# Kernel optimization log

Measured on AMD Instinct MI355X. Metric: run time of the kernel, lower is better.

The kernel has to match this reference:

```python
import jax, jax.numpy as jnp
import numpy as np

EPS = 1e-8
LN_EPS = 1e-5
CAPACITY_BETA = 1.5
IDEAL_CLASSES = 5.0

B, F, E, H, C, G = 8192, 1024, 30, 256, 100, 4096


def setup_inputs() -> dict:
    key = jax.random.key(0)
    ks = jax.random.split(key, 8)
    x = jax.random.normal(ks[0], (B, F), dtype=jnp.float32)
    prototypes = jax.random.normal(ks[1], (E, F), dtype=jnp.float32)
    g_new = jax.random.normal(ks[2], (G,), dtype=jnp.float32)
    g_mem = jax.random.normal(ks[3], (E, G), dtype=jnp.float32)
    class_counts = jax.random.randint(ks[4], (E,), 0, 12, dtype=jnp.int32)
    W1 = jax.random.normal(ks[5], (E, F, H), dtype=jnp.float32) * (1.0 / np.sqrt(F))
    b1 = jnp.zeros((E, H), dtype=jnp.float32)
    gamma = jnp.ones((E, H), dtype=jnp.float32)
    beta = jnp.zeros((E, H), dtype=jnp.float32)
    W2 = jax.random.normal(ks[6], (E, H, C), dtype=jnp.float32) * (1.0 / np.sqrt(H))
    b2 = jnp.zeros((E, C), dtype=jnp.float32)
    return {"x": x, "prototypes": prototypes, "g_new": g_new, "g_mem": g_mem,
            "class_counts": class_counts, "W1": W1, "b1": b1, "gamma": gamma,
            "beta": beta, "W2": W2, "b2": b2}


def _route_scores(x, prototypes, g_new, g_mem, class_counts):
    # Cosine similarity of each sample to each expert prototype: [B, E]
    xn = x / (jnp.linalg.norm(x, axis=-1, keepdims=True) + EPS)
    pn = prototypes / (jnp.linalg.norm(prototypes, axis=-1, keepdims=True) + EPS)
    sim = xn @ pn.T
    # Gradient alignment score per expert (cosine of new grad vs EMA memory), mapped to [0, 1]
    gn = g_new / (jnp.linalg.norm(g_new) + EPS)
    gm = g_mem / (jnp.linalg.norm(g_mem, axis=-1, keepdims=True) + EPS)
    align = 0.5 * (1.0 + gm @ gn)  # [E]
    # Capacity penalty: exponential decay once an expert exceeds its ideal class load
    overload = jnp.maximum(class_counts.astype(jnp.float32) / IDEAL_CLASSES - 1.0, 0.0)
    capacity = jnp.exp(-CAPACITY_BETA * overload)  # [E]
    return sim * (align * capacity)[None, :]  # [B, E]


def reference(x, prototypes, g_new, g_mem, class_counts, W1, b1, gamma, beta, W2, b2):
    scores = _route_scores(x, prototypes, g_new, g_mem, class_counts)  # [B, E]
    assign = jnp.argmax(scores, axis=-1)  # [B] expert id per sample
    # Expert MLP: Linear -> LayerNorm -> GELU -> Linear, evaluated for all experts
    h = jnp.einsum('bf,efh->ebh', x, W1) + b1[:, None, :]  # [E, B, H]
    mu = h.mean(axis=-1, keepdims=True)
    var = ((h - mu) ** 2).mean(axis=-1, keepdims=True)
    ln = (h - mu) * jax.lax.rsqrt(var + LN_EPS) * gamma[:, None, :] + beta[:, None, :]
    a = jax.nn.gelu(ln, approximate=False)  # torch nn.GELU default is exact erf
    logits_all = jnp.einsum('ebh,ehc->ebc', a, W2) + b2[:, None, :]  # [E, B, C]
    # Dispatch: each sample keeps only its assigned expert's logits
    logits = logits_all[assign, jnp.arange(x.shape[0])]  # [B, C]
    return logits
```

## Files before the change

### kernel.cpp

```cpp
#include <hip/hip_runtime.h>
#include <hip/hip_bf16.h>
#include <math.h>
#include <float.h>

namespace {
constexpr int Bn = 8192;
constexpr int Fn = 1024;
constexpr int En = 30;
constexpr int Hn = 256;
constexpr int Cn = 100;
constexpr int Gn = 4096;
constexpr int TILECAP64 = 158;
constexpr int TILECAP16 = 540;
constexpr float EPSF  = 1e-8f;
constexpr float LNEPS = 1e-5f;

typedef _Float16 f16x8 __attribute__((ext_vector_type(8)));
typedef float    f32x4 __attribute__((ext_vector_type(4)));

__device__ __forceinline__ int bswz(int k) { return (k & 7) ^ ((k >> 3) << 2); }
}

#define GLDS16(g, s) __builtin_amdgcn_global_load_lds(                         \
    (const __attribute__((address_space(1))) void*)(uintptr_t)(g),             \
    (__attribute__((address_space(3))) void*)(uintptr_t)(s), 16, 0, 0)

__global__ __launch_bounds__(256) void k_route_w(
    const float* __restrict__ protos,
    const float* __restrict__ g_new,
    const float* __restrict__ g_mem,
    const int* __restrict__ ccounts,
    float* __restrict__ w,
    int* __restrict__ cnt) {
  const int e = blockIdx.x, t = threadIdx.x;
  if (e == 0 && t < 32) cnt[t] = 0;
  float d = 0.f, gm2 = 0.f, gn2 = 0.f, p2 = 0.f;
  for (int g = t; g < Gn; g += 256) {
    float a = g_new[g];
    float m = g_mem[(size_t)e * Gn + g];
    d += a * m; gm2 += m * m; gn2 += a * a;
  }
  for (int f = t; f < Fn; f += 256) {
    float v = protos[(size_t)e * Fn + f];
    p2 += v * v;
  }
#pragma unroll
  for (int m = 1; m < 64; m <<= 1) {
    d   += __shfl_xor(d, m);
    gm2 += __shfl_xor(gm2, m);
    gn2 += __shfl_xor(gn2, m);
    p2  += __shfl_xor(p2, m);
  }
  __shared__ float red[4][4];
  const int lane = t & 63, wid = t >> 6;
  if (lane == 0) { red[wid][0] = d; red[wid][1] = gm2; red[wid][2] = gn2; red[wid][3] = p2; }
  __syncthreads();
  if (t == 0) {
    d   = red[0][0] + red[1][0] + red[2][0] + red[3][0];
    gm2 = red[0][1] + red[1][1] + red[2][1] + red[3][1];
    gn2 = red[0][2] + red[1][2] + red[2][2] + red[3][2];
    p2  = red[0][3] + red[1][3] + red[2][3] + red[3][3];
    float align = 0.5f * (1.0f + d / ((sqrtf(gm2) + EPSF) * (sqrtf(gn2) + EPSF)));
    float over  = fmaxf((float)ccounts[e] / 5.0f - 1.0f, 0.0f);
    float cap   = expf(-1.5f * over);
    w[e] = align * cap / (sqrtf(p2) + EPSF);
  }
}

__global__ __launch_bounds__(256) void k_scores_mfma(
    const float* __restrict__ x,
    const float* __restrict__ protos,
    const float* __restrict__ w,
    int* __restrict__ assign) {
  const int b0 = blockIdx.x * 16;
  extern __shared__ char smem[];
  __shared__ float av_[16][2];
  __shared__ int   ai_[16][2];
  const int t = threadIdx.x, l = t & 63, wv = t >> 6;
  const int nt = wv & 1;

  const char* asrc;
  {
    const int row = t >> 4, pos = t & 15;
    asrc = (const char*)x + (size_t)(b0 + row) * 4096 + (pos ^ (row & 7)) * 16;
  }
  const char* bsrc[2];
#pragma unroll
  for (int i = 0; i < 2; i++) {
    const int D = i * 256 + t, row = D >> 4, pos = D & 15;
    bsrc[i] = (const char*)protos + (size_t)min(row, En - 1) * 4096 +
              (pos ^ (row & 7)) * 16;
  }

  const int r15 = l & 15, kq = l >> 4;
  int addrA[2][2];
#pragma unroll
  for (int ks = 0; ks < 2; ks++)
#pragma unroll
    for (int i = 0; i < 2; i++)
      addrA[ks][i] = r15 * 256 + (((ks * 8 + kq * 2 + i) ^ (r15 & 7)) * 16);
  int addrB[2][2];
#pragma unroll
  for (int ks = 0; ks < 2; ks++)
#pragma unroll
    for (int i = 0; i < 2; i++) {
      const int er = nt * 16 + r15;
      addrB[ks][i] = 4096 + er * 256 + (((ks * 8 + kq * 2 + i) ^ (er & 7)) * 16);
    }

  const int  e_w   = nt * 16 + r15;
  const bool valid = (e_w < En);
  const float wsc  = w[min(e_w, En - 1)];

  f32x4 acc = (f32x4){0.f, 0.f, 0.f, 0.f};

  auto stage = [&](int buf, int kt) {
    char* bb = smem + buf * 12288;
    GLDS16(asrc + kt * 256, bb + wv * 1024);
#pragma unroll
    for (int i = 0; i < 2; i++)
      GLDS16(bsrc[i] + kt * 256, bb + 4096 + i * 4096 + wv * 1024);
  };

  stage(0, 0);
  __syncthreads();
  int cur = 0;
  for (int kt = 0; kt < 16; ++kt) {
    if (kt < 15) stage(cur ^ 1, kt + 1);
    const char* bb = smem + cur * 12288;
    if (wv < 2) {
#pragma unroll
      for (int ks = 0; ks < 2; ks++) {
        f16x8 ah, al;
        {
          float4 a0 = *(const float4*)(bb + addrA[ks][0]);
          float4 a1 = *(const float4*)(bb + addrA[ks][1]);
          float av[8] = {a0.x, a0.y, a0.z, a0.w, a1.x, a1.y, a1.z, a1.w};
#pragma unroll
          for (int j = 0; j < 8; j++) {
            _Float16 hh = (_Float16)av[j];
            ah[j] = hh;
            al[j] = (_Float16)(av[j] - (float)hh);
          }
        }
        f16x8 bh, bl;
        {
          float4 b0v = *(const float4*)(bb + addrB[ks][0]);
          float4 b1v = *(const float4*)(bb + addrB[ks][1]);
          float bv[8] = {b0v.x, b0v.y, b0v.z, b0v.w, b1v.x, b1v.y, b1v.z, b1v.w};
#pragma unroll
          for (int j = 0; j < 8; j++) {
            _Float16 hh = (_Float16)bv[j];
            bh[j] = hh;
            bl[j] = (_Float16)(bv[j] - (float)hh);
          }
        }
        acc = __builtin_amdgcn_mfma_f32_16x16x32_f16(ah, bh, acc, 0, 0, 0);
        acc = __builtin_amdgcn_mfma_f32_16x16x32_f16(al, bh, acc, 0, 0, 0);
        acc = __builtin_amdgcn_mfma_f32_16x16x32_f16(ah, bl, acc, 0, 0, 0);
        acc = __builtin_amdgcn_mfma_f32_16x16x32_f16(al, bl, acc, 0, 0, 0);
      }
    }
    __syncthreads();
    cur ^= 1;
  }

  if (wv < 2) {
#pragma unroll
    for (int j = 0; j < 4; j++) {
      float best = valid ? acc[j] * wsc : -FLT_MAX;
      int bi = e_w;
#pragma unroll
      for (int m = 1; m < 16; m <<= 1) {
        float ov = __shfl_xor(best, m);
        int   oi = __shfl_xor(bi, m);
        if (ov > best || (ov == best && oi < bi)) { best = ov; bi = oi; }
      }
      if (r15 == 0) {
        const int s = kq * 4 + j;
        av_[s][nt] = best;
        ai_[s][nt] = bi;
      }
    }
  }
  __syncthreads();
  if (t < 16) {
    const float v0 = av_[t][0], v1 = av_[t][1];
    assign[b0 + t] = (v1 > v0) ? ai_[t][1] : ai_[t][0];
  }
}

__global__ __launch_bounds__(256) void k_bucket(
    const int* __restrict__ assign,
    int* __restrict__ cnt,
    int* __restrict__ list) {
  __shared__ int lcnt[32], lbase[32];
  const int t = threadIdx.x;
  const int b = blockIdx.x * 256 + t;
  if (t < 32) lcnt[t] = 0;
  __syncthreads();
  const int e = assign[b];
  const int lpos = atomicAdd(&lcnt[e], 1);
  __syncthreads();
  if (t < 32) lbase[t] = (lcnt[t] > 0) ? atomicAdd(&cnt[t], lcnt[t]) : 0;
  __syncthreads();
  list[e * Bn + lbase[e] + lpos] = b;
}

__global__ __launch_bounds__(256) void k_planz(
    const int* __restrict__ cnt,
    int* __restrict__ tiles64,
    int* __restrict__ tiles16,
    float* __restrict__ hbuf) {
  const size_t i = ((size_t)blockIdx.x * 256 + threadIdx.x) * 4;
  *(float4*)(hbuf + i) = make_float4(0.f, 0.f, 0.f, 0.f);
  if (blockIdx.x == 0 && threadIdx.x == 0) {
    int tot = 0;
    for (int e = 0; e < En; e++) {
      int nt = (cnt[e] + 63) >> 6;
      for (int k = 0; k < nt && tot + k < TILECAP64; k++)
        tiles64[tot + k] = (e << 16) | k;
      tot += nt;
    }
    for (int k = tot; k < TILECAP64; k++) tiles64[k] = -1;
    tot = 0;
    for (int e = 0; e < En; e++) {
      int nt = (cnt[e] + 15) >> 4;
      for (int k = 0; k < nt && tot + k < TILECAP16; k++)
        tiles16[tot + k] = (e << 16) | k;
      tot += nt;
    }
    for (int k = tot; k < TILECAP16; k++) tiles16[k] = -1;
  }
}

__global__ __launch_bounds__(256) void k_l1_f16(
    const float* __restrict__ x,
    const float* __restrict__ W1,
    const float* __restrict__ b1,
    const int* __restrict__ cnt,
    const int* __restrict__ list,
    const int* __restrict__ tiles,
    float* __restrict__ hbuf) {
  const int tv = tiles[blockIdx.x];
  if (tv < 0) return;
  const int e = tv >> 16, ti = tv & 0xffff;
  const int n = cnt[e];
  const int s0 = ti * 64;
  const int ns = min(64, n - s0);
  const int h0 = blockIdx.y * 128;
  const int k0 = blockIdx.z * 16;

  extern __shared__ char smem[];
  __shared__ int idx[64];
  const int t = threadIdx.x, l = t & 63, w = t >> 6;
  if (t < 64) idx[t] = list[e * Bn + s0 + min(t, ns - 1)];
  __syncthreads();

  const char* asrc[2];
#pragma unroll
  for (int i = 0; i < 2; i++) {
    const int D = i * 256 + t, row = D >> 3, pos = D & 7;
    asrc[i] = (const char*)x + (size_t)idx[row] * 4096 + (pos ^ (row & 7)) * 16;
  }
  const char* bsrc[4];
#pragma unroll
  for (int i = 0; i < 4; i++) {
    const int k  = i * 8 + w * 2 + (l >> 5);
    const int c  = (l & 31) ^ bswz(k);
    bsrc[i] = (const char*)W1 +
              ((size_t)(e * Fn + k) * Hn + h0) * 4 + c * 16;
  }

  const int r15 = l & 15, kq = l >> 4;
  int addrA[4][2];
#pragma unroll
  for (int m = 0; m < 4; m++)
#pragma unroll
    for (int i = 0; i < 2; i++) {
      const int row = m * 16 + r15;
      addrA[m][i] = row * 128 + (((kq * 2 + i) ^ (row & 7)) * 16);
    }
  int addrB[2][8];
#pragma unroll
  for (int nn = 0; nn < 2; nn++)
#pragma unroll
    for (int j = 0; j < 8; j++) {
      const int h = w * 32 + nn * 16 + r15;
      const int kl = kq * 8 + j;
      addrB[nn][j] = 8192 + kl * 512 + (((h >> 2) ^ bswz(kl)) * 16) + (h & 3) * 4;
    }

  f32x4 acc[4][2];
#pragma unroll
  for (int m = 0; m < 4; m++)
#pragma unroll
    for (int nn = 0; nn < 2; nn++) acc[m][nn] = (f32x4){0.f, 0.f, 0.f, 0.f};

  auto stage = [&](int buf, int kt) {
    char* bb = smem + buf * 24576;
#pragma unroll
    for (int i = 0; i < 2; i++)
      GLDS16(asrc[i] + kt * 128, bb + i * 4096 + w * 1024);
#pragma unroll
    for (int i = 0; i < 4; i++)
      GLDS16(bsrc[i] + (size_t)kt * 32768, bb + 8192 + i * 4096 + w * 1024);
  };

  stage(0, k0);
  __syncthreads();
  int cur = 0;
  for (int kt = k0; kt < k0 + 16; ++kt) {
    if (kt < k0 + 15) stage(cur ^ 1, kt + 1);
    const char* bb = smem + cur * 24576;

    f16x8 ah[4], al[4];
#pragma unroll
    for (int m = 0; m < 4; m++) {
      float4 a0 = *(const float4*)(bb + addrA[m][0]);
      float4 a1 = *(const float4*)(bb + addrA[m][1]);
      float av[8] = {a0.x, a0.y, a0.z, a0.w, a1.x, a1.y, a1.z, a1.w};
#pragma unroll
      for (int j = 0; j < 8; j++) {
        _Float16 hh = (_Float16)av[j];
        ah[m][j] = hh;
        al[m][j] = (_Float16)(av[j] - (float)hh);
      }
    }
#pragma unroll
    for (int nn = 0; nn < 2; nn++) {
      float bv[8];
#pragma unroll
      for (int j = 0; j < 8; j++)
        bv[j] = *(const float*)(bb + addrB[nn][j]);
      f16x8 bh, bl;
#pragma unroll
      for (int j = 0; j < 8; j++) {
        _Float16 hh = (_Float16)bv[j];
        bh[j] = hh;
        bl[j] = (_Float16)(bv[j] - (float)hh);
      }
#pragma unroll
      for (int m = 0; m < 4; m++) {
        acc[m][nn] = __builtin_amdgcn_mfma_f32_16x16x32_f16(ah[m], bh, acc[m][nn], 0, 0, 0);
        acc[m][nn] = __builtin_amdgcn_mfma_f32_16x16x32_f16(al[m], bh, acc[m][nn], 0, 0, 0);
        acc[m][nn] = __builtin_amdgcn_mfma_f32_16x16x32_f16(ah[m], bl, acc[m][nn], 0, 0, 0);
      }
    }
    __syncthreads();
    cur ^= 1;
  }

  float bias[2];
#pragma unroll
  for (int nn = 0; nn < 2; nn++)
    bias[nn] = (blockIdx.z == 0)
             ? b1[(size_t)e * Hn + h0 + w * 32 + nn * 16 + r15] : 0.f;
#pragma unroll
  for (int m = 0; m < 4; m++) {
#pragma unroll
    for (int j = 0; j < 4; j++) {
      const int r = m * 16 + kq * 4 + j;
      if (r < ns) {
        float* dst = hbuf + (size_t)idx[r] * Hn + h0 + w * 32;
#pragma unroll
        for (int nn = 0; nn < 2; nn++)
          atomicAdd(dst + nn * 16 + r15, acc[m][nn][j] + bias[nn]);
      }
    }
  }
}

__global__ __launch_bounds__(256) void k_ln2_mfma(
    const float* __restrict__ hbuf,
    const float* __restrict__ gamma,
    const float* __restrict__ beta,
    const float* __restrict__ W2,
    const float* __restrict__ b2,
    const int* __restrict__ cnt,
    const int* __restrict__ list,
    const int* __restrict__ tiles16,
    float* __restrict__ out) {
  const int tv = tiles16[blockIdx.x];
  if (tv < 0) return;
  const int e = tv >> 16, ti = tv & 0xffff;
  const int n = cnt[e];
  const int s0 = ti * 16;
  const int ns = min(16, n - s0);

  __shared__ __align__(16) char aT[16 * 1024];
  __shared__ __align__(16) char bW[2][13312];
  __shared__ int idx[16];

  const int t = threadIdx.x, l = t & 63, w = t >> 6;
  if (t < 16) idx[t] = list[e * Bn + s0 + min(t, ns - 1)];

  const char* w2e = (const char*)W2 + (size_t)e * (Hn * Cn * 4);
  auto stageB = [&](int buf, int kt) {
    const int base = kt * 12800;
    for (int i = w; i < 13; i += 4) {
      int off = base + i * 1024 + l * 16;
      if (off > 102400 - 16) off = 102400 - 16;
      GLDS16(w2e + off, bW[buf] + i * 1024);
    }
  };

  stageB(0, 0);
  __syncthreads();

  const int s = t >> 4, seg = t & 15;
  const int b = idx[s];
  float hv[16];
  float sum = 0.f, sq = 0.f;
  {
    const float* src = hbuf + (size_t)b * Hn + seg * 16;
#pragma unroll
    for (int i = 0; i < 16; i += 4) {
      float4 v = *(const float4*)(src + i);
      hv[i] = v.x; hv[i+1] = v.y; hv[i+2] = v.z; hv[i+3] = v.w;
      sum += v.x + v.y + v.z + v.w;
      sq  += v.x*v.x + v.y*v.y + v.z*v.z + v.w*v.w;
    }
  }
#pragma unroll
  for (int m = 1; m < 16; m <<= 1) { sum += __shfl_xor(sum, m); sq += __shfl_xor(sq, m); }
  const float mu = sum * (1.f / 256.f);
  float var = fmaxf(sq * (1.f / 256.f) - mu * mu, 0.f);
  const float rstd = rsqrtf(var + LNEPS);
#pragma unroll
  for (int i4 = 0; i4 < 4; i4++) {
    float av[4];
#pragma unroll
    for (int j = 0; j < 4; j++) {
      const int hh = seg * 16 + i4 * 4 + j;
      const float g  = gamma[(size_t)e * Hn + hh];
      const float be = beta[(size_t)e * Hn + hh];
      const float ln = (hv[i4 * 4 + j] - mu) * rstd * g + be;
      av[j] = 0.5f * ln * (1.0f + erff(ln * 0.70710678118654752f));
    }
    const int chunk = (seg * 4 + i4) ^ (s & 7);
    *(float4*)(aT + s * 1024 + chunk * 16) = make_float4(av[0], av[1], av[2], av[3]);
  }

  const int r15 = l & 15, kq = l >> 4;
  int addrB[2][8];
#pragma unroll
  for (int ni = 0; ni < 2; ni++) {
    const int nt = w + ni * 4;
    const int c = nt * 16 + r15;
#pragma unroll
    for (int j = 0; j < 8; j++)
      addrB[ni][j] = ((kq * 8 + j) * Cn + c) * 4;
  }

  f32x4 acc[2];
  acc[0] = (f32x4){0.f, 0.f, 0.f, 0.f};
  acc[1] = (f32x4){0.f, 0.f, 0.f, 0.f};

  __syncthreads();

  int cur = 0;
  for (int kt = 0; kt < 8; ++kt) {
    if (kt < 7) stageB(cur ^ 1, kt + 1);

    f16x8 ah, al;
    {
      const int c0 = (kt * 8 + kq * 2) ^ (r15 & 7);
      const int c1 = (kt * 8 + kq * 2 + 1) ^ (r15 & 7);
      float4 a0 = *(const float4*)(aT + r15 * 1024 + c0 * 16);
      float4 a1 = *(const float4*)(aT + r15 * 1024 + c1 * 16);
      float av[8] = {a0.x, a0.y, a0.z, a0.w, a1.x, a1.y, a1.z, a1.w};
#pragma unroll
      for (int j = 0; j < 8; j++) {
        _Float16 hh = (_Float16)av[j];
        ah[j] = hh;
        al[j] = (_Float16)(av[j] - (float)hh);
      }
    }
#pragma unroll
    for (int ni = 0; ni < 2; ni++) {
      const int nt = w + ni * 4;
      if (nt < 7) {
        float bv[8];
#pragma unroll
        for (int j = 0; j < 8; j++)
          bv[j] = *(const float*)(bW[cur] + addrB[ni][j]);
        f16x8 bh, bl;
#pragma unroll
        for (int j = 0; j < 8; j++) {
          _Float16 hh = (_Float16)bv[j];
          bh[j] = hh;
          bl[j] = (_Float16)(bv[j] - (float)hh);
        }
        acc[ni] = __builtin_amdgcn_mfma_f32_16x16x32_f16(ah, bh, acc[ni], 0, 0, 0);
        acc[ni] = __builtin_amdgcn_mfma_f32_16x16x32_f16(al, bh, acc[ni], 0, 0, 0);
        acc[ni] = __builtin_amdgcn_mfma_f32_16x16x32_f16(ah, bl, acc[ni], 0, 0, 0);
      }
    }
    __syncthreads();
    cur ^= 1;
  }

#pragma unroll
  for (int ni = 0; ni < 2; ni++) {
    const int nt = w + ni * 4;
    if (nt >= 7) continue;
    const int c = nt * 16 + r15;
    if (c >= Cn) continue;
    const float bias = b2[(size_t)e * Cn + c];
#pragma unroll
    for (int j = 0; j < 4; j++) {
      const int r = kq * 4 + j;
      if (r < ns)
        out[(size_t)idx[r] * Cn + c] = acc[ni][j] + bias;
    }
  }
}

extern "C" void kernel_launch(void* const* d_in, const int* in_sizes, int n_in,
                              void* d_out, int out_size, void* d_ws, size_t ws_size,
                              hipStream_t stream) {
  const void* x       = d_in[0];
  const void* protos  = d_in[1];
  const void* g_new   = d_in[2];
  const void* g_mem   = d_in[3];
  const int*  ccounts = (const int*)d_in[4];
  const void* W1      = d_in[5];
  const void* b1      = d_in[6];
  const void* gamma   = d_in[7];
  const void* beta    = d_in[8];
  const void* W2      = d_in[9];
  const void* b2      = d_in[10];

  char* ws = (char*)d_ws;
  float* w       = (float*)(ws);
  int*   assign  = (int*)(ws + 512);
  int*   tiles64 = (int*)(ws + 512);
  int*   tiles16 = (int*)(ws + 512 + 1024);
  int*   cnt     = (int*)(ws + 512 + Bn * 4);
  int*   list    = (int*)(ws + 512 + Bn * 4 + 256);
  float* hbuf    = (float*)(ws + 1016576);

  k_route_w<<<dim3(En), 256, 0, stream>>>(
      (const float*)protos, (const float*)g_new, (const float*)g_mem,
      ccounts, w, cnt);
  k_scores_mfma<<<dim3(Bn / 16), 256, 24576, stream>>>(
      (const float*)x, (const float*)protos, w, assign);
  k_bucket<<<Bn / 256, 256, 0, stream>>>(assign, cnt, list);
  k_planz<<<dim3((Bn * Hn) / (256 * 4)), 256, 0, stream>>>(
      cnt, tiles64, tiles16, hbuf);
  k_l1_f16<<<dim3(TILECAP64, 2, 2), 256, 49152, stream>>>(
      (const float*)x, (const float*)W1, (const float*)b1,
      cnt, list, tiles64, hbuf);
  k_ln2_mfma<<<dim3(TILECAP16), 256, 0, stream>>>(
      hbuf, (const float*)gamma, (const float*)beta, (const float*)W2,
      (const float*)b2, cnt, list, tiles16, (float*)d_out);
}
```

Baseline: 222.0 us.

## Fold hbuf zeroing into scores kernel, parallelize plan, drop W1 low-half MFMA

Zeroing of the hidden buffer moves from the planning kernel into the scores kernel, so the plan kernel becomes a tiny one-block launch where two threads build the 64-row and 16-row tile lists in parallel. In the layer-1 GEMM the W1 operand is no longer split into high and low fp16 halves. It is converted with packed round-toward-zero conversion, which removes one of the three MFMAs per step and the split-conversion ALU work. This cuts compute and a large memory-zeroing pass, but lowers the precision of W1, which could affect accuracy.

```diff
diff --git a/kernel.cpp b/kernel.cpp
--- a/kernel.cpp
+++ b/kernel.cpp
@@ -16,9 +16,18 @@
 constexpr float LNEPS = 1e-5f;
 
 typedef _Float16 f16x8 __attribute__((ext_vector_type(8)));
+typedef __fp16   h16x2 __attribute__((ext_vector_type(2)));
 typedef float    f32x4 __attribute__((ext_vector_type(4)));
 
 __device__ __forceinline__ int bswz(int k) { return (k & 7) ^ ((k >> 3) << 2); }
+
+__device__ __forceinline__ f16x8 pk8(const float* v) {
+  union { h16x2 h2[4]; f16x8 v8; } u;
+#pragma unroll
+  for (int i = 0; i < 4; i++)
+    u.h2[i] = __builtin_amdgcn_cvt_pkrtz(v[2 * i], v[2 * i + 1]);
+  return u.v8;
+}
 }
 
 #define GLDS16(g, s) __builtin_amdgcn_global_load_lds(                         \
@@ -71,13 +80,21 @@
     const float* __restrict__ x,
     const float* __restrict__ protos,
     const float* __restrict__ w,
-    int* __restrict__ assign) {
+    int* __restrict__ assign,
+    float* __restrict__ hbuf) {
   const int b0 = blockIdx.x * 16;
   extern __shared__ char smem[];
   __shared__ float av_[16][2];
   __shared__ int   ai_[16][2];
   const int t = threadIdx.x, l = t & 63, wv = t >> 6;
   const int nt = wv & 1;
+
+  {
+    float* hz = hbuf + (size_t)blockIdx.x * 4096 + t * 4;
+#pragma unroll
+    for (int k = 0; k < 4; k++)
+      *(float4*)(hz + k * 1024) = make_float4(0.f, 0.f, 0.f, 0.f);
+  }
 
   const char* asrc;
   {
@@ -207,14 +224,11 @@
   list[e * Bn + lbase[e] + lpos] = b;
 }
 
-__global__ __launch_bounds__(256) void k_planz(
-    const int* __restrict__ cnt,
-    int* __restrict__ tiles64,
-    int* __restrict__ tiles16,
-    float* __restrict__ hbuf) {
-  const size_t i = ((size_t)blockIdx.x * 256 + threadIdx.x) * 4;
-  *(float4*)(hbuf + i) = make_float4(0.f, 0.f, 0.f, 0.f);
-  if (blockIdx.x == 0 && threadIdx.x == 0) {
+__global__ void k_plan(const int* __restrict__ cnt,
+                       int* __restrict__ tiles64,
+                       int* __restrict__ tiles16) {
+  const int t = threadIdx.x;
+  if (t == 0) {
     int tot = 0;
     for (int e = 0; e < En; e++) {
       int nt = (cnt[e] + 63) >> 6;
@@ -223,7 +237,8 @@
       tot += nt;
     }
     for (int k = tot; k < TILECAP64; k++) tiles64[k] = -1;
-    tot = 0;
+  } else if (t == 1) {
+    int tot = 0;
     for (int e = 0; e < En; e++) {
       int nt = (cnt[e] + 15) >> 4;
       for (int k = 0; k < nt && tot + k < TILECAP16; k++)
@@ -333,18 +348,11 @@
 #pragma unroll
       for (int j = 0; j < 8; j++)
         bv[j] = *(const float*)(bb + addrB[nn][j]);
-      f16x8 bh, bl;
-#pragma unroll
-      for (int j = 0; j < 8; j++) {
-        _Float16 hh = (_Float16)bv[j];
-        bh[j] = hh;
-        bl[j] = (_Float16)(bv[j] - (float)hh);
-      }
+      const f16x8 bh = pk8(bv);
 #pragma unroll
       for (int m = 0; m < 4; m++) {
         acc[m][nn] = __builtin_amdgcn_mfma_f32_16x16x32_f16(ah[m], bh, acc[m][nn], 0, 0, 0);
         acc[m][nn] = __builtin_amdgcn_mfma_f32_16x16x32_f16(al[m], bh, acc[m][nn], 0, 0, 0);
-        acc[m][nn] = __builtin_amdgcn_mfma_f32_16x16x32_f16(ah[m], bl, acc[m][nn], 0, 0, 0);
       }
     }
     __syncthreads();
@@ -545,10 +553,9 @@
       (const float*)protos, (const float*)g_new, (const float*)g_mem,
       ccounts, w, cnt);
   k_scores_mfma<<<dim3(Bn / 16), 256, 24576, stream>>>(
-      (const float*)x, (const float*)protos, w, assign);
+      (const float*)x, (const float*)protos, w, assign, hbuf);
   k_bucket<<<Bn / 256, 256, 0, stream>>>(assign, cnt, list);
-  k_planz<<<dim3((Bn * Hn) / (256 * 4)), 256, 0, stream>>>(
-      cnt, tiles64, tiles16, hbuf);
+  k_plan<<<1, 64, 0, stream>>>(cnt, tiles64, tiles16);
   k_l1_f16<<<dim3(TILECAP64, 2, 2), 256, 49152, stream>>>(
       (const float*)x, (const float*)W1, (const float*)b1,
       cnt, list, tiles64, hbuf);
```

After: 219.3 us. About the same (-1.2%).
